# Kernel optimization log

Measured on AMD Instinct MI355X. Metric: run time of the kernel, lower is better.

Reference implementation:

```python
import jax, jax.numpy as jnp
import numpy as np

TEMPERATURE = 0.1
NEG_INF = -1e30  # finite sentinel so masked logsumexp has zero (not NaN) gradient


def setup_inputs() -> dict:
    key = jax.random.key(0)
    k1, k2, k3 = jax.random.split(key, 3)
    N, D = 8192, 512          # flattened (batch * TRs) trials, feature dim
    NUM_CLASSES = 3           # vigilance states
    return {
        "objs_feats": jax.random.normal(k1, (N, D), dtype=jnp.float32),
        "objs_labels": jax.random.randint(k2, (N,), 0, NUM_CLASSES, dtype=jnp.int32),
        "bad_tr": jax.random.randint(k3, (N,), 0, 2, dtype=jnp.int32),
    }


def reference(objs_feats, objs_labels, bad_tr):
    # Faithful vectorization of SetCriterion.contrastive_loss_batch_without_break.
    N = objs_feats.shape[0]
    f = objs_feats / jnp.linalg.norm(objs_feats, axis=-1, keepdims=True)
    S = (f @ f.T) / TEMPERATURE                      # [N, N] cosine-sim logits

    valid = bad_tr == 0                              # [N]
    same = objs_labels[:, None] == objs_labels[None, :]
    eye = jnp.eye(N, dtype=bool)
    neg_mask = valid[None, :] & (~same)              # [N, N] negatives per anchor
    pos_mask = valid[None, :] & same & (~eye)        # [N, N] positives per anchor

    has_neg = neg_mask.any(axis=1)
    has_pos = pos_mask.any(axis=1)
    processed = valid & has_neg                      # anchors the loop doesn't `continue` past

    # logsumexp over negatives of each anchor row
    neg_lse = jax.nn.logsumexp(jnp.where(neg_mask, S, NEG_INF), axis=1)  # [N]

    # anchors WITH positives: CE over rows [S[i,p], S[i, negs...]] with target 0,
    # averaged over positives p -> mean_p( logaddexp(S[i,p], neg_lse_i) - S[i,p] )
    ce_per_pos = jnp.logaddexp(S, neg_lse[:, None]) - S                  # [N, N]
    pos_cnt = pos_mask.sum(axis=1)
    loss_with_pos = jnp.where(pos_mask, ce_per_pos, 0.0).sum(axis=1) / jnp.maximum(pos_cnt, 1)

    # anchors WITHOUT positives: pos logit is the constant 1/temperature
    inv_t = jnp.float32(1.0 / TEMPERATURE)
    loss_no_pos = jnp.logaddexp(inv_t, neg_lse) - inv_t

    per_anchor = jnp.where(has_pos, loss_with_pos, loss_no_pos)
    total = jnp.where(processed, per_anchor, 0.0).sum()
    # valid_obj_cnt starts at 1; no-pos anchors net to 0 (−1 then +1)
    count = 1 + (processed & has_pos).sum()
    return total / count.astype(total.dtype)
```

## Files before the change

### kernel.cpp

```cpp
#include <hip/hip_runtime.h>

typedef __bf16 bf16x8 __attribute__((ext_vector_type(8)));
typedef __bf16 bf16x4 __attribute__((ext_vector_type(4)));
typedef float f32x4 __attribute__((ext_vector_type(4)));

#define GLOAD_LDS16(g, l)                                                      \
  __builtin_amdgcn_global_load_lds(                                            \
      (const __attribute__((address_space(1))) void*)(g),                      \
      (__attribute__((address_space(3))) void*)(l), 16, 0, 0)


__global__ __launch_bounds__(1024) void k_scan(
    const int* __restrict__ labels, const int* __restrict__ bad,
    unsigned char* __restrict__ code, int* __restrict__ dst,
    int* __restrict__ hdr, __bf16* __restrict__ fng,
    unsigned char* __restrict__ gcode, float* __restrict__ out, int Nv,
    int Dv) {
  const int t = threadIdx.x;
  const int lane = t & 63, wv = t >> 6;
  const int per = Nv >> 10;
  const int base = t * per;
  unsigned char lc[8];
  int cnt[3] = {0, 0, 0};
  for (int k = 0; k < per; ++k) {
    const int r = base + k;
    const unsigned char c =
        (bad[r] == 0) ? (unsigned char)labels[r] : (unsigned char)255;
    lc[k] = c;
    code[r] = c;
    if (c <= 2) cnt[c]++;
  }
  int inc0 = cnt[0], inc1 = cnt[1], inc2 = cnt[2];
#pragma unroll
  for (int off = 1; off < 64; off <<= 1) {
    const int a = __shfl_up(inc0, off);
    const int b = __shfl_up(inc1, off);
    const int c = __shfl_up(inc2, off);
    if (lane >= off) {
      inc0 += a;
      inc1 += b;
      inc2 += c;
    }
  }
  __shared__ int wt[16][3], wo[17][3];
  if (lane == 63) {
    wt[wv][0] = inc0;
    wt[wv][1] = inc1;
    wt[wv][2] = inc2;
  }
  __syncthreads();
  if (t == 0) {
    int s0 = 0, s1 = 0, s2 = 0;
    for (int w = 0; w < 16; ++w) {
      wo[w][0] = s0;
      wo[w][1] = s1;
      wo[w][2] = s2;
      s0 += wt[w][0];
      s1 += wt[w][1];
      s2 += wt[w][2];
    }
    wo[16][0] = s0;
    wo[16][1] = s1;
    wo[16][2] = s2;
  }
  __syncthreads();
  const int C0 = wo[16][0], C1 = wo[16][1], C2 = wo[16][2];
  int run[3];
  run[0] = wo[wv][0] + inc0 - cnt[0];
  run[1] = C0 + wo[wv][1] + inc1 - cnt[1];
  run[2] = C0 + C1 + wo[wv][2] + inc2 - cnt[2];
  for (int k = 0; k < per; ++k) {
    const int c = lc[k];
    dst[base + k] = (c <= 2) ? run[c]++ : -1;
  }
  const int M = C0 + C1 + C2;
  const int Mpad = (M + 127) & ~127;
  if (t == 0) {
    const int NTv = Mpad >> 7;
    hdr[0] = M;
    hdr[1] = Mpad;
    hdr[2] = NTv;
    hdr[3] = NTv * (NTv + 1) / 2;
    hdr[4] = C0;
    hdr[5] = C1;
    hdr[6] = C2;
    int count = 1;
    if (C0 >= 2 && M > C0) count += C0;
    if (C1 >= 2 && M > C1) count += C1;
    if (C2 >= 2 && M > C2) count += C2;
    hdr[7] = count;
    out[0] = 0.f;
  }
  for (int i = M + t; i < Mpad; i += 1024) gcode[i] = 255;
  const int nv4 = (Mpad - M) * (Dv >> 3);
  float4* fp = (float4*)(fng + (size_t)M * Dv);
  const float4 z = {0.f, 0.f, 0.f, 0.f};
  for (int i = t; i < nv4; i += 1024) fp[i] = z;
}

__global__ __launch_bounds__(512) void k_norm(const float* __restrict__ X,
                                              const unsigned char* __restrict__
                                                  code,
                                              const int* __restrict__ dst,
                                              __bf16* __restrict__ fng,
                                              unsigned char* __restrict__ gcode,
                                              int Nv, int Dv) {
  const int t = threadIdx.x;
  const int tl = t & 63;
  const int row = blockIdx.x * 8 + (t >> 6);
  if (row >= Nv) return;
  const unsigned char c = code[row];
  if (c > 2) return;
  const float4* xr = (const float4*)(X + (size_t)row * Dv);
  if (Dv == 512) {
    const float4 v0 = xr[tl * 2];
    const float4 v1 = xr[tl * 2 + 1];
    float ss = v0.x * v0.x + v0.y * v0.y + v0.z * v0.z + v0.w * v0.w +
               v1.x * v1.x + v1.y * v1.y + v1.z * v1.z + v1.w * v1.w;
#pragma unroll
    for (int off = 1; off < 64; off <<= 1) ss += __shfl_xor(ss, off);
    const float inv = 1.0f / sqrtf(ss);
    const int g = dst[row];
    bf16x8 o;
    o[0] = (__bf16)(v0.x * inv);
    o[1] = (__bf16)(v0.y * inv);
    o[2] = (__bf16)(v0.z * inv);
    o[3] = (__bf16)(v0.w * inv);
    o[4] = (__bf16)(v1.x * inv);
    o[5] = (__bf16)(v1.y * inv);
    o[6] = (__bf16)(v1.z * inv);
    o[7] = (__bf16)(v1.w * inv);
    *(bf16x8*)(fng + (size_t)g * Dv + tl * 8) = o;
    if (tl == 0) gcode[g] = c;
    return;
  }
  float ss = 0.f;
  for (int idx = tl; idx < (Dv >> 2); idx += 64) {
    const float4 v = xr[idx];
    ss += v.x * v.x + v.y * v.y + v.z * v.z + v.w * v.w;
  }
#pragma unroll
  for (int off = 1; off < 64; off <<= 1) ss += __shfl_xor(ss, off);
  const float inv = 1.0f / sqrtf(ss);
  const int g = dst[row];
  for (int idx = tl; idx < (Dv >> 3); idx += 64) {
    const float4 u0 = xr[idx * 2];
    const float4 u1 = xr[idx * 2 + 1];
    bf16x8 o;
    o[0] = (__bf16)(u0.x * inv);
    o[1] = (__bf16)(u0.y * inv);
    o[2] = (__bf16)(u0.z * inv);
    o[3] = (__bf16)(u0.w * inv);
    o[4] = (__bf16)(u1.x * inv);
    o[5] = (__bf16)(u1.y * inv);
    o[6] = (__bf16)(u1.z * inv);
    o[7] = (__bf16)(u1.w * inv);
    *(bf16x8*)(fng + (size_t)g * Dv + idx * 8) = o;
  }
  if (tl == 0) gcode[g] = c;
}

__device__ __forceinline__ void tri_decode(int blk, int NT, int& bi, int& bj) {
  int b = 0, rem = blk, span = NT;
  while (rem >= span) {
    rem -= span;
    b++;
    span--;
  }
  bi = b;
  bj = b + rem;
}

__device__ __forceinline__ int xcd_swz(int w, int n) {
  const int q = n >> 3, r = n & 7, x = w & 7, o = w >> 3;
  return (x < r ? x * (q + 1) : r * (q + 1) + (x - r) * q) + o;
}

__device__ __forceinline__ bool tile_overlap(const unsigned char* gcode,
                                             size_t sA, int lastA,
                                             size_t rowB) {
  const int la0 = gcode[sA], la1 = gcode[sA + lastA];
  const int lb0 = gcode[rowB], lb1 = gcode[rowB + 127];
  const int hiA = la1 > 2 ? 2 : la1;
  const int hiB = lb1 > 2 ? 2 : lb1;
  const int lo = la0 > lb0 ? la0 : lb0;
  const int hi = hiA < hiB ? hiA : hiB;
  return (la0 <= 2) && (lb0 <= 2) && (lo <= hi);
}

__global__ __launch_bounds__(512, 6) void k_p1(
    const __bf16* __restrict__ fng, const unsigned char* __restrict__ gcode,
    const int* __restrict__ hdr, float* __restrict__ P,
    _Float16* __restrict__ Sc, int Nv, int Dv) {
  const int NTv = hdr[2];
  const int ntri = hdr[3];
  int bid = blockIdx.x;
  if (bid >= ntri) return;
  bid = xcd_swz(bid, ntri);
  int bi, bj;
  tri_decode(bid, NTv, bi, bj);
  const size_t sA = (size_t)bi * 128;
  const size_t rowB = (size_t)bj * 128;
  __shared__ __align__(16) __bf16 As[2][128 * 32];
  __shared__ __align__(16) __bf16 Bs[2][128 * 32];

  const int t = threadIdx.x;
  const int lane = t & 63;
  const int wave = t >> 6;
  const int quad = lane >> 4;
  const int l16 = lane & 15;
  const int wr = (wave >> 1) * 32;
  const int wc = (wave & 1) * 64;
  const int r4 = t >> 2, q4 = t & 3;

  f32x4 acc[2][4] = {};
  auto stage = [&](int k0, int b) {
    GLOAD_LDS16(fng + (sA + r4) * Dv + k0 + q4 * 8,
                &As[b][(size_t)wave * 64 * 8]);
    GLOAD_LDS16(fng + (rowB + r4) * Dv + k0 + q4 * 8,
                &Bs[b][(size_t)wave * 64 * 8]);
  };
  stage(0, 0);
  int buf = 0;
  for (int k0 = 0; k0 < Dv; k0 += 32) {
    __syncthreads();
    if (k0 + 32 < Dv) stage(k0 + 32, buf ^ 1);
    bf16x8 af[2], bfv[4];
#pragma unroll
    for (int mi = 0; mi < 2; ++mi)
      af[mi] = *(const bf16x8*)&As[buf][(wr + mi * 16 + l16) * 32 + quad * 8];
#pragma unroll
    for (int ni = 0; ni < 4; ++ni)
      bfv[ni] = *(const bf16x8*)&Bs[buf][(wc + ni * 16 + l16) * 32 + quad * 8];
#pragma unroll
    for (int mi = 0; mi < 2; ++mi)
#pragma unroll
      for (int ni = 0; ni < 4; ++ni)
        acc[mi][ni] = __builtin_amdgcn_mfma_f32_16x16x32_bf16(
            af[mi], bfv[ni], acc[mi][ni], 0, 0, 0);
    buf ^= 1;
  }
  unsigned char ca[8], cb[4];
#pragma unroll
  for (int mi = 0; mi < 2; ++mi)
#pragma unroll
    for (int r = 0; r < 4; ++r)
      ca[mi * 4 + r] = gcode[sA + wr + mi * 16 + quad * 4 + r];
#pragma unroll
  for (int ni = 0; ni < 4; ++ni) cb[ni] = gcode[rowB + wc + ni * 16 + l16];
  const bool ov = tile_overlap(gcode, sA, 127, rowB);
  _Float16* St = Sc + (size_t)bid * 16384;

  float rowsum[8] = {};
  float colsum[4] = {};
#pragma unroll
  for (int mi = 0; mi < 2; ++mi)
#pragma unroll
    for (int ni = 0; ni < 4; ++ni)
#pragma unroll
      for (int r = 0; r < 4; ++r) {
        const float s = acc[mi][ni][r] * 10.0f;
        const float ex = __expf(s);
        const int a = ca[mi * 4 + r], b = cb[ni];
        const bool diff = a != b;
        rowsum[mi * 4 + r] += (b <= 2 && diff) ? ex : 0.f;
        colsum[ni] += (a <= 2 && diff) ? ex : 0.f;
        if (ov)
          St[(wr + mi * 16 + quad * 4 + r) * 128 + wc + ni * 16 + l16] =
              (_Float16)s;
      }
#pragma unroll
  for (int off = 1; off < 16; off <<= 1)
#pragma unroll
    for (int k = 0; k < 8; ++k) rowsum[k] += __shfl_xor(rowsum[k], off);
  if (l16 == 0) {
    const int sreal = bj * 4 + (wave & 1);
    const int szero = bj * 4 + 2 + (wave & 1);
    const size_t r0 = sA + wr + quad * 4;
    float4 v0 = {rowsum[0], rowsum[1], rowsum[2], rowsum[3]};
    float4 v1 = {rowsum[4], rowsum[5], rowsum[6], rowsum[7]};
    const float4 z = {0.f, 0.f, 0.f, 0.f};
    *(float4*)(P + (size_t)sreal * Nv + r0) = v0;
    *(float4*)(P + (size_t)sreal * Nv + r0 + 16) = v1;
    *(float4*)(P + (size_t)szero * Nv + r0) = z;
    *(float4*)(P + (size_t)szero * Nv + r0 + 16) = z;
  }
  if (bi != bj) {
#pragma unroll
    for (int off = 16; off < 64; off <<= 1)
#pragma unroll
      for (int ni = 0; ni < 4; ++ni) colsum[ni] += __shfl_xor(colsum[ni], off);
    if (quad == 0) {
      const int s = bi * 4 + (wave >> 1);
#pragma unroll
      for (int ni = 0; ni < 4; ++ni)
        P[(size_t)s * Nv + rowB + wc + ni * 16 + l16] = colsum[ni];
    }
  }
}

__global__ __launch_bounds__(256) void k_red(const float* __restrict__ P,
                                             float* __restrict__ out,
                                             const int* __restrict__ hdr,
                                             int Nv) {
  const int g = blockIdx.x * 256 + threadIdx.x;
  if (g >= Nv || g >= hdr[1]) return;
  const int ns = hdr[2] * 4;
  float s0 = 0.f, s1 = 0.f, s2 = 0.f, s3 = 0.f;
  int k = 0;
  for (; k + 4 <= ns; k += 4) {
    s0 += P[(size_t)k * Nv + g];
    s1 += P[(size_t)(k + 1) * Nv + g];
    s2 += P[(size_t)(k + 2) * Nv + g];
    s3 += P[(size_t)(k + 3) * Nv + g];
  }
  for (; k < ns; ++k) s0 += P[(size_t)k * Nv + g];
  out[g] = (s0 + s1) + (s2 + s3);
}

__global__ __launch_bounds__(256) void k_p2(
    const unsigned char* __restrict__ gcode, const int* __restrict__ hdr,
    const float* __restrict__ E, float* __restrict__ P2,
    const _Float16* __restrict__ Sc, int Nv) {
  const int NTv = hdr[2];
  if ((int)blockIdx.x >= hdr[3]) return;
  int bi, bj;
  tri_decode(blockIdx.x, NTv, bi, bj);
  const int h = blockIdx.y;
  const size_t sA = (size_t)bi * 128 + h * 64;
  const size_t rowB = (size_t)bj * 128;
  const int t = threadIdx.x;
  const bool diag = (bi == bj);

  if (!tile_overlap(gcode, sA, 63, rowB)) {
    if (t < 64) {
      const size_t r = sA + t;
      P2[(size_t)(bj * 4 + 0) * Nv + r] = 0.f;
      P2[(size_t)(bj * 4 + 1) * Nv + r] = 0.f;
      P2[(size_t)(bj * 4 + 2) * Nv + r] = 0.f;
      P2[(size_t)(bj * 4 + 3) * Nv + r] = 0.f;
    } else if (t < 192 && !diag) {
      const size_t r = rowB + t - 64;
      P2[(size_t)(bi * 4 + h * 2) * Nv + r] = 0.f;
      P2[(size_t)(bi * 4 + h * 2 + 1) * Nv + r] = 0.f;
    }
    return;
  }

  const _Float16* St = Sc + ((size_t)blockIdx.x * 2 + h) * 8192;
  const int l8 = t & 15;
  unsigned char cb[8];
  float eB[8];
  {
    const uint2 cv = *(const uint2*)(gcode + rowB + l8 * 8);
    const unsigned char* cp = (const unsigned char*)&cv;
#pragma unroll
    for (int e = 0; e < 8; ++e) cb[e] = cp[e];
    const float4 e0 = *(const float4*)(E + rowB + l8 * 8);
    const float4 e1 = *(const float4*)(E + rowB + l8 * 8 + 4);
    eB[0] = e0.x; eB[1] = e0.y; eB[2] = e0.z; eB[3] = e0.w;
    eB[4] = e1.x; eB[5] = e1.y; eB[6] = e1.z; eB[7] = e1.w;
  }
  float colsum[8] = {};
#pragma unroll
  for (int k = 0; k < 4; ++k) {
    const int row = k * 16 + (t >> 4);
    const int a = gcode[sA + row];
    const float eA = E[sA + row];
    const float4 sv = *(const float4*)(St + row * 128 + l8 * 8);
    const _Float16* hp = (const _Float16*)&sv;
    float rsum = 0.f;
#pragma unroll
    for (int e = 0; e < 8; ++e) {
      const int col = l8 * 8 + e;
      const float em = __expf(-(float)hp[e]);
      const bool pos =
          (a == cb[e]) && (cb[e] <= 2) && !(diag && (row + h * 64) == col);
      rsum += pos ? __logf(1.f + eA * em) : 0.f;
      colsum[e] += pos ? __logf(1.f + eB[e] * em) : 0.f;
    }
#pragma unroll
    for (int off = 1; off < 16; off <<= 1) rsum += __shfl_xor(rsum, off);
    if (l8 == 0) {
      const size_t r = sA + row;
      P2[(size_t)(bj * 4 + h * 2) * Nv + r] = rsum;
      P2[(size_t)(bj * 4 + h * 2 + 1) * Nv + r] = 0.f;
      P2[(size_t)(bj * 4 + (1 - h) * 2) * Nv + r] = 0.f;
      P2[(size_t)(bj * 4 + (1 - h) * 2 + 1) * Nv + r] = 0.f;
    }
  }
  __shared__ float colpart[128 * 17];
#pragma unroll
  for (int e = 0; e < 8; ++e) colpart[(l8 * 8 + e) * 17 + (t >> 4)] = colsum[e];
  __syncthreads();
  if (t < 128 && !diag) {
    float cs = 0.f;
#pragma unroll
    for (int i = 0; i < 16; ++i) cs += colpart[t * 17 + i];
    const size_t r = rowB + t;
    P2[(size_t)(bi * 4 + h * 2) * Nv + r] = cs;
    P2[(size_t)(bi * 4 + h * 2 + 1) * Nv + r] = 0.f;
  }
}

__global__ __launch_bounds__(256) void k_fin(const float* __restrict__ P2,
                                             const float* __restrict__ E,
                                             const unsigned char* __restrict__
                                                 gcode,
                                             const int* __restrict__ hdr,
                                             float* __restrict__ out, int Nv) {
  const int g = blockIdx.x * 256 + threadIdx.x;
  const int t = threadIdx.x;
  float contrib = 0.f;
  if (g < hdr[1]) {
    const int l = gcode[g];
    if (l <= 2) {
      const int c0 = hdr[4], c1 = hdr[5], c2 = hdr[6];
      const int vt = c0 + c1 + c2;
      const int cmy = (l == 0) ? c0 : ((l == 1) ? c1 : c2);
      if (vt - cmy > 0) {
        const int pos_cnt = cmy - 1;
        if (pos_cnt > 0) {
          const int ns = hdr[2] * 4;
          float s0 = 0.f, s1 = 0.f, s2 = 0.f, s3 = 0.f;
          int k = 0;
          for (; k + 4 <= ns; k += 4) {
            s0 += P2[(size_t)k * Nv + g];
            s1 += P2[(size_t)(k + 1) * Nv + g];
            s2 += P2[(size_t)(k + 2) * Nv + g];
            s3 += P2[(size_t)(k + 3) * Nv + g];
          }
          for (; k < ns; ++k) s0 += P2[(size_t)k * Nv + g];
          contrib = ((s0 + s1) + (s2 + s3)) / (float)pos_cnt;
        } else {
          contrib = __logf(1.f + E[g] * __expf(-10.0f));
        }
      }
    }
  }
#pragma unroll
  for (int off = 32; off; off >>= 1) contrib += __shfl_down(contrib, off);
  __shared__ float sd[4];
  if ((t & 63) == 0) sd[t >> 6] = contrib;
  __syncthreads();
  if (t == 0) {
    const float tot = sd[0] + sd[1] + sd[2] + sd[3];
    atomicAdd(out, tot / (float)hdr[7]);
  }
}

extern "C" void kernel_launch(void* const* d_in, const int* in_sizes, int n_in,
                              void* d_out, int out_size, void* d_ws,
                              size_t ws_size, hipStream_t stream) {
  const float* X = (const float*)d_in[0];
  const int* labels = (const int*)d_in[1];
  const int* bad = (const int*)d_in[2];
  const int Nv = in_sizes[1];
  const int Dv = in_sizes[0] / Nv;

  size_t off = 0;
  auto alloc = [&](size_t bytes) -> void* {
    size_t p = (off + 255) & ~(size_t)255;
    off = p + bytes;
    return (void*)((char*)d_ws + p);
  };
  const int NT = Nv / 128;
  const int ntri_max = NT * (NT + 1) / 2;
  __bf16* fng = (__bf16*)alloc((size_t)Nv * Dv * 2);
  float* P = (float*)alloc((size_t)Nv * 256 * 4);
  float* P2 = (float*)alloc((size_t)Nv * 256 * 4);
  _Float16* Sc = (_Float16*)alloc((size_t)ntri_max * 2 * 8192 * 2);
  float* E = (float*)alloc((size_t)Nv * 4);
  int* dst = (int*)alloc((size_t)Nv * 4);
  unsigned char* code = (unsigned char*)alloc((size_t)Nv);
  unsigned char* gcode = (unsigned char*)alloc((size_t)Nv);
  int* hdr = (int*)alloc(64);
  if (off > ws_size) return;
  float* outp = (float*)d_out;

  k_scan<<<1, 1024, 0, stream>>>(labels, bad, code, dst, hdr, fng, gcode,
                                 outp, Nv, Dv);
  k_norm<<<(Nv + 7) / 8, 512, 0, stream>>>(X, code, dst, fng, gcode, Nv, Dv);
  k_p1<<<ntri_max, 512, 0, stream>>>(fng, gcode, hdr, P, Sc, Nv, Dv);
  k_red<<<(Nv + 255) / 256, 256, 0, stream>>>(P, E, hdr, Nv);
  dim3 gp(ntri_max, 2);
  k_p2<<<gp, 256, 0, stream>>>(gcode, hdr, E, P2, Sc, Nv);
  k_fin<<<(Nv + 255) / 256, 256, 0, stream>>>(P2, E, gcode, hdr, outp, Nv);
}
```

Before: 135.1 us.

## Fuse reduction, pass-2 and final sum into one triangle-tile kernel

Removes the k_red and k_fin kernels and the P2 partial buffer. Each pass-2 block now recomputes the per-row negative sums for its 256 rows (A and B tiles) straight from P into shared memory. It processes a full 128x128 tile instead of two 64-row halves, and accumulates the normalized loss contribution directly into the output with one atomic per block. This saves two launches and the P2 write/read traffic, at the cost of redundant column reductions of P in every tile and many more atomics. It also adds an XCD swizzle of block indices.

Result: faster. 125.6 us (-7.0%).

```diff
diff --git a/kernel.cpp b/kernel.cpp
--- a/kernel.cpp
+++ b/kernel.cpp
@@ -299,75 +299,65 @@
   }
 }
 
-__global__ __launch_bounds__(256) void k_red(const float* __restrict__ P,
-                                             float* __restrict__ out,
-                                             const int* __restrict__ hdr,
-                                             int Nv) {
-  const int g = blockIdx.x * 256 + threadIdx.x;
-  if (g >= Nv || g >= hdr[1]) return;
-  const int ns = hdr[2] * 4;
-  float s0 = 0.f, s1 = 0.f, s2 = 0.f, s3 = 0.f;
-  int k = 0;
-  for (; k + 4 <= ns; k += 4) {
-    s0 += P[(size_t)k * Nv + g];
-    s1 += P[(size_t)(k + 1) * Nv + g];
-    s2 += P[(size_t)(k + 2) * Nv + g];
-    s3 += P[(size_t)(k + 3) * Nv + g];
-  }
-  for (; k < ns; ++k) s0 += P[(size_t)k * Nv + g];
-  out[g] = (s0 + s1) + (s2 + s3);
-}
-
 __global__ __launch_bounds__(256) void k_p2(
     const unsigned char* __restrict__ gcode, const int* __restrict__ hdr,
-    const float* __restrict__ E, float* __restrict__ P2,
-    const _Float16* __restrict__ Sc, int Nv) {
+    const float* __restrict__ P, const _Float16* __restrict__ Sc,
+    float* __restrict__ out, int Nv) {
   const int NTv = hdr[2];
-  if ((int)blockIdx.x >= hdr[3]) return;
+  const int ntri = hdr[3];
+  if ((int)blockIdx.x >= ntri) return;
+  const int bid = xcd_swz(blockIdx.x, ntri);
   int bi, bj;
-  tri_decode(blockIdx.x, NTv, bi, bj);
-  const int h = blockIdx.y;
-  const size_t sA = (size_t)bi * 128 + h * 64;
+  tri_decode(bid, NTv, bi, bj);
+  const size_t sA = (size_t)bi * 128;
   const size_t rowB = (size_t)bj * 128;
   const int t = threadIdx.x;
   const bool diag = (bi == bj);
-
-  if (!tile_overlap(gcode, sA, 63, rowB)) {
-    if (t < 64) {
-      const size_t r = sA + t;
-      P2[(size_t)(bj * 4 + 0) * Nv + r] = 0.f;
-      P2[(size_t)(bj * 4 + 1) * Nv + r] = 0.f;
-      P2[(size_t)(bj * 4 + 2) * Nv + r] = 0.f;
-      P2[(size_t)(bj * 4 + 3) * Nv + r] = 0.f;
-    } else if (t < 192 && !diag) {
-      const size_t r = rowB + t - 64;
-      P2[(size_t)(bi * 4 + h * 2) * Nv + r] = 0.f;
-      P2[(size_t)(bi * 4 + h * 2 + 1) * Nv + r] = 0.f;
-    }
-    return;
-  }
-
-  const _Float16* St = Sc + ((size_t)blockIdx.x * 2 + h) * 8192;
+  if (!tile_overlap(gcode, sA, 127, rowB)) return;
+
+  const int c0 = hdr[4], c1 = hdr[5], c2 = hdr[6];
+  const int vt = c0 + c1 + c2;
+  __shared__ float E_s[256];
+  __shared__ float colpart[128 * 17];
+  __shared__ float sd[4];
+
+  {
+    const int ns = NTv * 4;
+    const size_t g = (t < 128) ? (sA + t) : (rowB + (t - 128));
+    float s0 = 0.f, s1 = 0.f, s2 = 0.f, s3 = 0.f;
+    int k = 0;
+    for (; k + 4 <= ns; k += 4) {
+      s0 += P[(size_t)k * Nv + g];
+      s1 += P[(size_t)(k + 1) * Nv + g];
+      s2 += P[(size_t)(k + 2) * Nv + g];
+      s3 += P[(size_t)(k + 3) * Nv + g];
+    }
+    for (; k < ns; ++k) s0 += P[(size_t)k * Nv + g];
+    E_s[t] = (s0 + s1) + (s2 + s3);
+  }
+  __syncthreads();
+
+  const _Float16* St = Sc + (size_t)bid * 16384;
   const int l8 = t & 15;
-  unsigned char cb[8];
+  const int rg = t >> 4;
+  unsigned char cbv[8];
   float eB[8];
   {
     const uint2 cv = *(const uint2*)(gcode + rowB + l8 * 8);
     const unsigned char* cp = (const unsigned char*)&cv;
 #pragma unroll
-    for (int e = 0; e < 8; ++e) cb[e] = cp[e];
-    const float4 e0 = *(const float4*)(E + rowB + l8 * 8);
-    const float4 e1 = *(const float4*)(E + rowB + l8 * 8 + 4);
-    eB[0] = e0.x; eB[1] = e0.y; eB[2] = e0.z; eB[3] = e0.w;
-    eB[4] = e1.x; eB[5] = e1.y; eB[6] = e1.z; eB[7] = e1.w;
+    for (int e = 0; e < 8; ++e) cbv[e] = cp[e];
+#pragma unroll
+    for (int e = 0; e < 8; ++e) eB[e] = E_s[128 + l8 * 8 + e];
   }
   float colsum[8] = {};
-#pragma unroll
-  for (int k = 0; k < 4; ++k) {
-    const int row = k * 16 + (t >> 4);
+  float part = 0.f;
+#pragma unroll
+  for (int k = 0; k < 8; ++k) {
+    const int row = k * 16 + rg;
     const int a = gcode[sA + row];
-    const float eA = E[sA + row];
-    const float4 sv = *(const float4*)(St + row * 128 + l8 * 8);
+    const float eA = E_s[row];
+    const float4 sv = *(const float4*)(St + (size_t)row * 128 + l8 * 8);
     const _Float16* hp = (const _Float16*)&sv;
     float rsum = 0.f;
 #pragma unroll
@@ -375,73 +365,41 @@
       const int col = l8 * 8 + e;
       const float em = __expf(-(float)hp[e]);
       const bool pos =
-          (a == cb[e]) && (cb[e] <= 2) && !(diag && (row + h * 64) == col);
+          (a == cbv[e]) && (cbv[e] <= 2) && !(diag && row == col);
       rsum += pos ? __logf(1.f + eA * em) : 0.f;
       colsum[e] += pos ? __logf(1.f + eB[e] * em) : 0.f;
     }
 #pragma unroll
     for (int off = 1; off < 16; off <<= 1) rsum += __shfl_xor(rsum, off);
-    if (l8 == 0) {
-      const size_t r = sA + row;
-      P2[(size_t)(bj * 4 + h * 2) * Nv + r] = rsum;
-      P2[(size_t)(bj * 4 + h * 2 + 1) * Nv + r] = 0.f;
-      P2[(size_t)(bj * 4 + (1 - h) * 2) * Nv + r] = 0.f;
-      P2[(size_t)(bj * 4 + (1 - h) * 2 + 1) * Nv + r] = 0.f;
-    }
-  }
-  __shared__ float colpart[128 * 17];
-#pragma unroll
-  for (int e = 0; e < 8; ++e) colpart[(l8 * 8 + e) * 17 + (t >> 4)] = colsum[e];
+    if (l8 == 0 && a <= 2) {
+      const int cmy = (a == 0) ? c0 : ((a == 1) ? c1 : c2);
+      if (vt - cmy > 0 && cmy >= 2) part += rsum / (float)(cmy - 1);
+    }
+  }
+#pragma unroll
+  for (int e = 0; e < 8; ++e) colpart[(l8 * 8 + e) * 17 + rg] = colsum[e];
   __syncthreads();
   if (t < 128 && !diag) {
     float cs = 0.f;
 #pragma unroll
     for (int i = 0; i < 16; ++i) cs += colpart[t * 17 + i];
-    const size_t r = rowB + t;
-    P2[(size_t)(bi * 4 + h * 2) * Nv + r] = cs;
-    P2[(size_t)(bi * 4 + h * 2 + 1) * Nv + r] = 0.f;
-  }
-}
-
-__global__ __launch_bounds__(256) void k_fin(const float* __restrict__ P2,
-                                             const float* __restrict__ E,
-                                             const unsigned char* __restrict__
-                                                 gcode,
-                                             const int* __restrict__ hdr,
-                                             float* __restrict__ out, int Nv) {
-  const int g = blockIdx.x * 256 + threadIdx.x;
-  const int t = threadIdx.x;
-  float contrib = 0.f;
-  if (g < hdr[1]) {
-    const int l = gcode[g];
-    if (l <= 2) {
-      const int c0 = hdr[4], c1 = hdr[5], c2 = hdr[6];
-      const int vt = c0 + c1 + c2;
-      const int cmy = (l == 0) ? c0 : ((l == 1) ? c1 : c2);
-      if (vt - cmy > 0) {
-        const int pos_cnt = cmy - 1;
-        if (pos_cnt > 0) {
-          const int ns = hdr[2] * 4;
-          float s0 = 0.f, s1 = 0.f, s2 = 0.f, s3 = 0.f;
-          int k = 0;
-          for (; k + 4 <= ns; k += 4) {
-            s0 += P2[(size_t)k * Nv + g];
-            s1 += P2[(size_t)(k + 1) * Nv + g];
-            s2 += P2[(size_t)(k + 2) * Nv + g];
-            s3 += P2[(size_t)(k + 3) * Nv + g];
-          }
-          for (; k < ns; ++k) s0 += P2[(size_t)k * Nv + g];
-          contrib = ((s0 + s1) + (s2 + s3)) / (float)pos_cnt;
-        } else {
-          contrib = __logf(1.f + E[g] * __expf(-10.0f));
-        }
-      }
-    }
-  }
-#pragma unroll
-  for (int off = 32; off; off >>= 1) contrib += __shfl_down(contrib, off);
-  __shared__ float sd[4];
-  if ((t & 63) == 0) sd[t >> 6] = contrib;
+    const int b = gcode[rowB + t];
+    if (b <= 2) {
+      const int cmy = (b == 0) ? c0 : ((b == 1) ? c1 : c2);
+      if (vt - cmy > 0 && cmy >= 2) part += cs / (float)(cmy - 1);
+    }
+  }
+  if (diag && t < 128) {
+    const int a = gcode[sA + t];
+    if (a <= 2) {
+      const int cmy = (a == 0) ? c0 : ((a == 1) ? c1 : c2);
+      if (vt - cmy > 0 && cmy == 1)
+        part += __logf(1.f + E_s[t] * __expf(-10.0f));
+    }
+  }
+#pragma unroll
+  for (int off = 32; off; off >>= 1) part += __shfl_down(part, off);
+  if ((t & 63) == 0) sd[t >> 6] = part;
   __syncthreads();
   if (t == 0) {
     const float tot = sd[0] + sd[1] + sd[2] + sd[3];
@@ -468,9 +426,7 @@
   const int ntri_max = NT * (NT + 1) / 2;
   __bf16* fng = (__bf16*)alloc((size_t)Nv * Dv * 2);
   float* P = (float*)alloc((size_t)Nv * 256 * 4);
-  float* P2 = (float*)alloc((size_t)Nv * 256 * 4);
-  _Float16* Sc = (_Float16*)alloc((size_t)ntri_max * 2 * 8192 * 2);
-  float* E = (float*)alloc((size_t)Nv * 4);
+  _Float16* Sc = (_Float16*)alloc((size_t)ntri_max * 16384 * 2);
   int* dst = (int*)alloc((size_t)Nv * 4);
   unsigned char* code = (unsigned char*)alloc((size_t)Nv);
   unsigned char* gcode = (unsigned char*)alloc((size_t)Nv);
@@ -482,8 +438,5 @@
                                  outp, Nv, Dv);
   k_norm<<<(Nv + 7) / 8, 512, 0, stream>>>(X, code, dst, fng, gcode, Nv, Dv);
   k_p1<<<ntri_max, 512, 0, stream>>>(fng, gcode, hdr, P, Sc, Nv, Dv);
-  k_red<<<(Nv + 255) / 256, 256, 0, stream>>>(P, E, hdr, Nv);
-  dim3 gp(ntri_max, 2);
-  k_p2<<<gp, 256, 0, stream>>>(gcode, hdr, E, P2, Sc, Nv);
-  k_fin<<<(Nv + 255) / 256, 256, 0, stream>>>(P2, E, gcode, hdr, outp, Nv);
-}
+  k_p2<<<ntri_max, 256, 0, stream>>>(gcode, hdr, P, Sc, outp, Nv);
+}
```
